# Kernel optimization log

Hardware: AMD Instinct MI355X
Metric: run time of the kernel (lower is better)

Reference implementation:

```python
import jax, jax.numpy as jnp
import numpy as np
from jax import lax

H = 128


def _ema_scan(x):
    # x: [B, T, N, F] -> EMA along T: s_t = 0.9*s_{t-1} + 0.1*x_t
    xt = jnp.moveaxis(x, 1, 0)  # [T, B, N, F]

    def step(s, xi):
        s = s * 0.9 + xi * 0.1
        return s, s

    _, ys = lax.scan(step, jnp.zeros_like(xt[0]), xt)
    return jnp.moveaxis(ys, 0, 1)  # [B, T, N, F]


def setup_inputs() -> dict:
    key = jax.random.key(0)
    k1, k2, k3, k4, k5 = jax.random.split(key, 5)
    B, T, N = 4, 96, 512
    x = jax.random.normal(k1, (B, T, N, H), dtype=jnp.float32)
    s = 1.0 / np.sqrt(H)
    W_exp = jax.random.uniform(k2, (2 * H, H), jnp.float32, -s, s)
    b_exp = jax.random.uniform(k3, (2 * H,), jnp.float32, -s, s)
    W_con = jax.random.uniform(k4, (H, H), jnp.float32, -s, s)
    b_con = jax.random.uniform(k5, (H,), jnp.float32, -s, s)
    return {"spatial_temporal_representation": x, "W_exp": W_exp, "b_exp": b_exp,
            "W_con": W_con, "b_con": b_con}


def reference(spatial_temporal_representation, W_exp, b_exp, W_con, b_con):
    x = spatial_temporal_representation  # [B,T,N,H]
    expanded = jnp.einsum('btnh,oh->btno', x, W_exp) + b_exp  # [B,T,N,2H]
    state_primary, state_gating = jnp.split(expanded, 2, axis=-1)
    gated_activation = jax.nn.sigmoid(_ema_scan(state_gating))
    out = jnp.einsum('btnh,oh->btno', state_primary * gated_activation, W_con) + b_con
    return out
```

## Files before the change

kernel.cpp:

```cpp
#include <hip/hip_runtime.h>

#define B_DIM 4
#define T_DIM 96
#define N_DIM 512
#define H_DIM 128
#define NH    (N_DIM * H_DIM)

#define WS_WEXP  0
#define WS_WCON  32768
#define WS_L     49152
#define WS_TOTAL 58368

typedef __attribute__((ext_vector_type(8))) short short8;
typedef __attribute__((ext_vector_type(4))) float f32x4;

__device__ __forceinline__ unsigned short f2b_rh(float f) {
    union { float f; unsigned u; } c; c.f = f;
    return (unsigned short)((c.u + 0x8000u) >> 16);
}
__device__ __forceinline__ unsigned pack_bf16_2(float a, float b) {
    union { float f; unsigned u; } ca, cb; ca.f = a; cb.f = b;
    return __builtin_amdgcn_perm(cb.u + 0x8000u, ca.u + 0x8000u, 0x07060302u);
}
__device__ __forceinline__ float u2f(unsigned u) {
    union { unsigned u; float f; } c; c.u = u;
    return c.f;
}

extern "C" __global__ void prep_kernel(const float* __restrict__ Wexp,
                                       const float* __restrict__ Wcon,
                                       unsigned short* __restrict__ ws) {
    int i = blockIdx.x * 256 + threadIdx.x;
    if (i < 32768) {
        ws[WS_WEXP + i] = f2b_rh(Wexp[i]);
    } else if (i < 49152) {
        int j = i - 32768;
        ws[WS_WCON + j] = f2b_rh(Wcon[j]);
    } else if (i < WS_TOTAL) {
        int j = i - 49152;
        int t = j / 96, k = j - t * 96;
        float v = 0.0f;
        if (k <= t) v = 0.1f * __expf((float)(t - k) * -0.1053605157f);
        ws[WS_L + j] = f2b_rh(v);
    }
}

extern "C" __global__ __launch_bounds__(256, 3)
void mamba_fused(const float* __restrict__ x,
                 const unsigned short* __restrict__ ws,
                 const float* __restrict__ b_exp,
                 const float* __restrict__ b_con,
                 float* __restrict__ out)
{
    __shared__ __align__(16) unsigned short gateT[H_DIM * 104];
    __shared__ __align__(16) unsigned short xpg[T_DIM * 136];

    const int tid  = threadIdx.x;
    const int wave = tid >> 6;
    const int lane = tid & 63;
    const int q    = lane >> 4;
    const int l16  = lane & 15;

    const int blk = blockIdx.x;
    const int n   = blk & (N_DIM - 1);
    const int b   = blk >> 9;

    const float* xg = x + ((size_t)b * T_DIM * N_DIM + (size_t)n) * H_DIM;

    {
        const int r2    = lane >> 5;
        const int c     = lane & 31;
        const int rbase = wave * 2 + r2;
        #pragma unroll
        for (int i = 0; i < 12; ++i) {
            const int r = i * 8 + rbase;
            float4 v = *(const float4*)(xg + (size_t)r * NH + c * 4);
            union { unsigned u[2]; ushort4 s; } pk;
            pk.u[0] = pack_bf16_2(v.x, v.y);
            pk.u[1] = pack_bf16_2(v.z, v.w);
            *(ushort4*)&xpg[r * 136 + c * 4] = pk.s;
        }
    }

    short8 wp[2][4], wg[2][4];
    #pragma unroll
    for (int ot = 0; ot < 2; ++ot) {
        const unsigned short* wrp = ws + WS_WEXP + (size_t)((wave * 2 + ot) * 16 + l16) * H_DIM + q * 8;
        #pragma unroll
        for (int k0 = 0; k0 < 4; ++k0) {
            wp[ot][k0] = *(const short8*)(wrp + k0 * 32);
            wg[ot][k0] = *(const short8*)(wrp + 128 * H_DIM + k0 * 32);
        }
    }
    __syncthreads();

    unsigned pacc[2][6][2];

    #pragma unroll
    for (int mt = 0; mt < 6; ++mt) {
        short8 bfr[4];
        #pragma unroll
        for (int k0 = 0; k0 < 4; ++k0)
            bfr[k0] = *(const short8*)&xpg[(mt * 16 + l16) * 136 + k0 * 32 + q * 8];
        f32x4 ap0 = {0.f,0.f,0.f,0.f}, ap1 = {0.f,0.f,0.f,0.f};
        f32x4 ag0 = {0.f,0.f,0.f,0.f}, ag1 = {0.f,0.f,0.f,0.f};
        #pragma unroll
        for (int k0 = 0; k0 < 4; ++k0) {
            ap0 = __builtin_amdgcn_mfma_f32_16x16x32_bf16(wp[0][k0], bfr[k0], ap0, 0, 0, 0);
            ap1 = __builtin_amdgcn_mfma_f32_16x16x32_bf16(wp[1][k0], bfr[k0], ap1, 0, 0, 0);
            ag0 = __builtin_amdgcn_mfma_f32_16x16x32_bf16(wg[0][k0], bfr[k0], ag0, 0, 0, 0);
            ag1 = __builtin_amdgcn_mfma_f32_16x16x32_bf16(wg[1][k0], bfr[k0], ag1, 0, 0, 0);
        }
        pacc[0][mt][0] = pack_bf16_2(ap0[0], ap0[1]);
        pacc[0][mt][1] = pack_bf16_2(ap0[2], ap0[3]);
        pacc[1][mt][0] = pack_bf16_2(ap1[0], ap1[1]);
        pacc[1][mt][1] = pack_bf16_2(ap1[2], ap1[3]);
        unsigned short* gr0 = &gateT[((wave * 2 + 0) * 16 + q * 4) * 104 + mt * 16 + l16];
        gr0[0]       = f2b_rh(ag0[0]);
        gr0[104]     = f2b_rh(ag0[1]);
        gr0[2 * 104] = f2b_rh(ag0[2]);
        gr0[3 * 104] = f2b_rh(ag0[3]);
        unsigned short* gr1 = &gateT[((wave * 2 + 1) * 16 + q * 4) * 104 + mt * 16 + l16];
        gr1[0]       = f2b_rh(ag1[0]);
        gr1[104]     = f2b_rh(ag1[1]);
        gr1[2 * 104] = f2b_rh(ag1[2]);
        gr1[3 * 104] = f2b_rh(ag1[3]);
    }

    asm volatile("s_waitcnt lgkmcnt(0)" ::: "memory");
    __builtin_amdgcn_sched_barrier(0);

    f32x4 eacc[2][6];
    #pragma unroll
    for (int ht = 0; ht < 2; ++ht)
        #pragma unroll
        for (int tt = 0; tt < 6; ++tt)
            eacc[ht][tt] = (f32x4){0.f, 0.f, 0.f, 0.f};
    {
        const unsigned short* wsL = ws + WS_L;
        #pragma unroll
        for (int kf = 0; kf < 3; ++kf) {
            short8 af0 = *(const short8*)&gateT[((wave * 2 + 0) * 16 + l16) * 104 + kf * 32 + q * 8];
            short8 af1 = *(const short8*)&gateT[((wave * 2 + 1) * 16 + l16) * 104 + kf * 32 + q * 8];
            #pragma unroll
            for (int tt = 0; tt < 6; ++tt) {
                if (tt < 2 * kf) continue;
                short8 bf = *(const short8*)(wsL + (size_t)(tt * 16 + l16) * 96 + kf * 32 + q * 8);
                eacc[0][tt] = __builtin_amdgcn_mfma_f32_16x16x32_bf16(af0, bf, eacc[0][tt], 0, 0, 0);
                eacc[1][tt] = __builtin_amdgcn_mfma_f32_16x16x32_bf16(af1, bf, eacc[1][tt], 0, 0, 0);
            }
        }
    }

    short8 wc[2][4];
    float4 bias2[2], bp[2], bgv[2];
    #pragma unroll
    for (int ot = 0; ot < 2; ++ot) {
        const int o = (wave * 2 + ot) * 16;
        const unsigned short* wrc = ws + WS_WCON + (size_t)(o + l16) * H_DIM + q * 8;
        #pragma unroll
        for (int k0 = 0; k0 < 4; ++k0)
            wc[ot][k0] = *(const short8*)(wrc + k0 * 32);
        bias2[ot] = *(const float4*)(b_con + o + q * 4);
        bp[ot]    = *(const float4*)(b_exp + o + q * 4);
        bgv[ot]   = *(const float4*)(b_exp + 128 + o + q * 4);
    }
    __syncthreads();

    #pragma unroll
    for (int ot = 0; ot < 2; ++ot) {
        const int hb = (wave * 2 + ot) * 16 + q * 4;
        #pragma unroll
        for (int tt = 0; tt < 6; ++tt) {
            const int t = tt * 16 + l16;
            const float c = 1.0f - __expf((float)(t + 1) * -0.1053605157f);
            f32x4 s = eacc[ot][tt];
            float sg0 = __fdividef(1.f, 1.f + __expf(-(s[0] + bgv[ot].x * c)));
            float sg1 = __fdividef(1.f, 1.f + __expf(-(s[1] + bgv[ot].y * c)));
            float sg2 = __fdividef(1.f, 1.f + __expf(-(s[2] + bgv[ot].z * c)));
            float sg3 = __fdividef(1.f, 1.f + __expf(-(s[3] + bgv[ot].w * c)));
            unsigned u0 = pacc[ot][tt][0], u1 = pacc[ot][tt][1];
            float p0 = (u2f(u0 << 16)         + bp[ot].x) * sg0;
            float p1 = (u2f(u0 & 0xffff0000u) + bp[ot].y) * sg1;
            float p2 = (u2f(u1 << 16)         + bp[ot].z) * sg2;
            float p3 = (u2f(u1 & 0xffff0000u) + bp[ot].w) * sg3;
            union { unsigned u[2]; ushort4 s; } pk;
            pk.u[0] = pack_bf16_2(p0, p1);
            pk.u[1] = pack_bf16_2(p2, p3);
            *(ushort4*)&xpg[t * 136 + hb] = pk.s;
        }
    }
    __syncthreads();

    float* og = out + ((size_t)b * T_DIM * N_DIM + (size_t)n) * H_DIM;
    #pragma unroll
    for (int mt = 0; mt < 6; ++mt) {
        short8 bfr[4];
        const unsigned short* prow = &xpg[(mt * 16 + l16) * 136];
        #pragma unroll
        for (int k0 = 0; k0 < 4; ++k0)
            bfr[k0] = *(const short8*)(prow + k0 * 32 + q * 8);
        const int t = mt * 16 + l16;
        #pragma unroll
        for (int ot = 0; ot < 2; ++ot) {
            f32x4 acc = {0.f, 0.f, 0.f, 0.f};
            #pragma unroll
            for (int k0 = 0; k0 < 4; ++k0)
                acc = __builtin_amdgcn_mfma_f32_16x16x32_bf16(wc[ot][k0], bfr[k0], acc, 0, 0, 0);
            const int o = (wave * 2 + ot) * 16 + q * 4;
            float4 v;
            v.x = acc[0] + bias2[ot].x;
            v.y = acc[1] + bias2[ot].y;
            v.z = acc[2] + bias2[ot].z;
            v.w = acc[3] + bias2[ot].w;
            *(float4*)(og + (size_t)t * NH + o) = v;
        }
    }
}

extern "C" void kernel_launch(void* const* d_in, const int* in_sizes, int n_in,
                              void* d_out, int out_size, void* d_ws, size_t ws_size,
                              hipStream_t stream) {
    const float* x     = (const float*)d_in[0];
    const float* W_exp = (const float*)d_in[1];
    const float* b_exp = (const float*)d_in[2];
    const float* W_con = (const float*)d_in[3];
    const float* b_con = (const float*)d_in[4];
    float* out = (float*)d_out;
    unsigned short* ws = (unsigned short*)d_ws;

    hipLaunchKernelGGL(prep_kernel, dim3(WS_TOTAL / 256), dim3(256), 0, stream,
                       W_exp, W_con, ws);
    hipLaunchKernelGGL(mamba_fused, dim3(B_DIM * N_DIM), dim3(256), 0, stream,
                       x, ws, b_exp, b_con, out);
}
```

Measured before the change: 224.7 us.

## Interleave gate projection with EMA matmul using small per-wave swizzled LDS buffer

```diff
diff --git a/kernel.cpp b/kernel.cpp
--- a/kernel.cpp
+++ b/kernel.cpp
@@ -45,15 +45,15 @@
     }
 }
 
-extern "C" __global__ __launch_bounds__(256, 3)
+extern "C" __global__ __launch_bounds__(256, 4)
 void mamba_fused(const float* __restrict__ x,
                  const unsigned short* __restrict__ ws,
                  const float* __restrict__ b_exp,
                  const float* __restrict__ b_con,
                  float* __restrict__ out)
 {
-    __shared__ __align__(16) unsigned short gateT[H_DIM * 104];
     __shared__ __align__(16) unsigned short xpg[T_DIM * 136];
+    __shared__ __align__(16) unsigned short gbuf[4 * 32 * 40];
 
     const int tid  = threadIdx.x;
     const int wave = tid >> 6;
@@ -95,60 +95,62 @@
     __syncthreads();
 
     unsigned pacc[2][6][2];
-
-    #pragma unroll
-    for (int mt = 0; mt < 6; ++mt) {
-        short8 bfr[4];
-        #pragma unroll
-        for (int k0 = 0; k0 < 4; ++k0)
-            bfr[k0] = *(const short8*)&xpg[(mt * 16 + l16) * 136 + k0 * 32 + q * 8];
-        f32x4 ap0 = {0.f,0.f,0.f,0.f}, ap1 = {0.f,0.f,0.f,0.f};
-        f32x4 ag0 = {0.f,0.f,0.f,0.f}, ag1 = {0.f,0.f,0.f,0.f};
-        #pragma unroll
-        for (int k0 = 0; k0 < 4; ++k0) {
-            ap0 = __builtin_amdgcn_mfma_f32_16x16x32_bf16(wp[0][k0], bfr[k0], ap0, 0, 0, 0);
-            ap1 = __builtin_amdgcn_mfma_f32_16x16x32_bf16(wp[1][k0], bfr[k0], ap1, 0, 0, 0);
-            ag0 = __builtin_amdgcn_mfma_f32_16x16x32_bf16(wg[0][k0], bfr[k0], ag0, 0, 0, 0);
-            ag1 = __builtin_amdgcn_mfma_f32_16x16x32_bf16(wg[1][k0], bfr[k0], ag1, 0, 0, 0);
-        }
-        pacc[0][mt][0] = pack_bf16_2(ap0[0], ap0[1]);
-        pacc[0][mt][1] = pack_bf16_2(ap0[2], ap0[3]);
-        pacc[1][mt][0] = pack_bf16_2(ap1[0], ap1[1]);
-        pacc[1][mt][1] = pack_bf16_2(ap1[2], ap1[3]);
-        unsigned short* gr0 = &gateT[((wave * 2 + 0) * 16 + q * 4) * 104 + mt * 16 + l16];
-        gr0[0]       = f2b_rh(ag0[0]);
-        gr0[104]     = f2b_rh(ag0[1]);
-        gr0[2 * 104] = f2b_rh(ag0[2]);
-        gr0[3 * 104] = f2b_rh(ag0[3]);
-        unsigned short* gr1 = &gateT[((wave * 2 + 1) * 16 + q * 4) * 104 + mt * 16 + l16];
-        gr1[0]       = f2b_rh(ag1[0]);
-        gr1[104]     = f2b_rh(ag1[1]);
-        gr1[2 * 104] = f2b_rh(ag1[2]);
-        gr1[3 * 104] = f2b_rh(ag1[3]);
-    }
-
-    asm volatile("s_waitcnt lgkmcnt(0)" ::: "memory");
-    __builtin_amdgcn_sched_barrier(0);
-
     f32x4 eacc[2][6];
     #pragma unroll
     for (int ht = 0; ht < 2; ++ht)
         #pragma unroll
         for (int tt = 0; tt < 6; ++tt)
             eacc[ht][tt] = (f32x4){0.f, 0.f, 0.f, 0.f};
-    {
-        const unsigned short* wsL = ws + WS_L;
-        #pragma unroll
-        for (int kf = 0; kf < 3; ++kf) {
-            short8 af0 = *(const short8*)&gateT[((wave * 2 + 0) * 16 + l16) * 104 + kf * 32 + q * 8];
-            short8 af1 = *(const short8*)&gateT[((wave * 2 + 1) * 16 + l16) * 104 + kf * 32 + q * 8];
+
+    const unsigned short* wsL = ws + WS_L;
+    unsigned short* gw = gbuf + wave * 1280;
+
+    #pragma unroll
+    for (int kf = 0; kf < 3; ++kf) {
+        #pragma unroll
+        for (int m01 = 0; m01 < 2; ++m01) {
+            const int mt = kf * 2 + m01;
+            short8 bfr[4];
             #pragma unroll
-            for (int tt = 0; tt < 6; ++tt) {
-                if (tt < 2 * kf) continue;
-                short8 bf = *(const short8*)(wsL + (size_t)(tt * 16 + l16) * 96 + kf * 32 + q * 8);
-                eacc[0][tt] = __builtin_amdgcn_mfma_f32_16x16x32_bf16(af0, bf, eacc[0][tt], 0, 0, 0);
-                eacc[1][tt] = __builtin_amdgcn_mfma_f32_16x16x32_bf16(af1, bf, eacc[1][tt], 0, 0, 0);
+            for (int k0 = 0; k0 < 4; ++k0)
+                bfr[k0] = *(const short8*)&xpg[(mt * 16 + l16) * 136 + k0 * 32 + q * 8];
+            f32x4 ap0 = {0.f,0.f,0.f,0.f}, ap1 = {0.f,0.f,0.f,0.f};
+            f32x4 ag0 = {0.f,0.f,0.f,0.f}, ag1 = {0.f,0.f,0.f,0.f};
+            #pragma unroll
+            for (int k0 = 0; k0 < 4; ++k0) {
+                ap0 = __builtin_amdgcn_mfma_f32_16x16x32_bf16(wp[0][k0], bfr[k0], ap0, 0, 0, 0);
+                ap1 = __builtin_amdgcn_mfma_f32_16x16x32_bf16(wp[1][k0], bfr[k0], ap1, 0, 0, 0);
+                ag0 = __builtin_amdgcn_mfma_f32_16x16x32_bf16(wg[0][k0], bfr[k0], ag0, 0, 0, 0);
+                ag1 = __builtin_amdgcn_mfma_f32_16x16x32_bf16(wg[1][k0], bfr[k0], ag1, 0, 0, 0);
             }
+            pacc[0][mt][0] = pack_bf16_2(ap0[0], ap0[1]);
+            pacc[0][mt][1] = pack_bf16_2(ap0[2], ap0[3]);
+            pacc[1][mt][0] = pack_bf16_2(ap1[0], ap1[1]);
+            pacc[1][mt][1] = pack_bf16_2(ap1[2], ap1[3]);
+            const int cw = (m01 * 16 + l16) ^ ((q >> 1) << 4);
+            unsigned short* g0 = gw + (q * 4) * 40 + cw;
+            unsigned short* g1 = g0 + 16 * 40;
+            g0[0]      = f2b_rh(ag0[0]);
+            g0[40]     = f2b_rh(ag0[1]);
+            g0[2 * 40] = f2b_rh(ag0[2]);
+            g0[3 * 40] = f2b_rh(ag0[3]);
+            g1[0]      = f2b_rh(ag1[0]);
+            g1[40]     = f2b_rh(ag1[1]);
+            g1[2 * 40] = f2b_rh(ag1[2]);
+            g1[3 * 40] = f2b_rh(ag1[3]);
+        }
+        asm volatile("s_waitcnt lgkmcnt(0)" ::: "memory");
+        __builtin_amdgcn_sched_barrier(0);
+
+        const int cr = (q * 8) ^ ((l16 >> 3) << 4);
+        short8 af0 = *(const short8*)&gw[l16 * 40 + cr];
+        short8 af1 = *(const short8*)&gw[(16 + l16) * 40 + cr];
+        #pragma unroll
+        for (int tt = 0; tt < 6; ++tt) {
+            if (tt < 2 * kf) continue;
+            short8 bf = *(const short8*)(wsL + (size_t)(tt * 16 + l16) * 96 + kf * 32 + q * 8);
+            eacc[0][tt] = __builtin_amdgcn_mfma_f32_16x16x32_bf16(af0, bf, eacc[0][tt], 0, 0, 0);
+            eacc[1][tt] = __builtin_amdgcn_mfma_f32_16x16x32_bf16(af1, bf, eacc[1][tt], 0, 0, 0);
         }
     }
 
```

Result: slower. 261.3 us (+16.3%).

## Load x directly into MFMA fragments and merge LDS buffers for higher occupancy

Applied to the files above, without the earlier changes.

```diff
diff --git a/kernel.cpp b/kernel.cpp
--- a/kernel.cpp
+++ b/kernel.cpp
@@ -45,15 +45,14 @@
     }
 }
 
-extern "C" __global__ __launch_bounds__(256, 3)
+extern "C" __global__ __launch_bounds__(256, 4)
 void mamba_fused(const float* __restrict__ x,
                  const unsigned short* __restrict__ ws,
                  const float* __restrict__ b_exp,
                  const float* __restrict__ b_con,
                  float* __restrict__ out)
 {
-    __shared__ __align__(16) unsigned short gateT[H_DIM * 104];
-    __shared__ __align__(16) unsigned short xpg[T_DIM * 136];
+    __shared__ __align__(16) unsigned short gpg[128 * 104];
 
     const int tid  = threadIdx.x;
     const int wave = tid >> 6;
@@ -67,21 +66,6 @@
 
     const float* xg = x + ((size_t)b * T_DIM * N_DIM + (size_t)n) * H_DIM;
 
-    {
-        const int r2    = lane >> 5;
-        const int c     = lane & 31;
-        const int rbase = wave * 2 + r2;
-        #pragma unroll
-        for (int i = 0; i < 12; ++i) {
-            const int r = i * 8 + rbase;
-            float4 v = *(const float4*)(xg + (size_t)r * NH + c * 4);
-            union { unsigned u[2]; ushort4 s; } pk;
-            pk.u[0] = pack_bf16_2(v.x, v.y);
-            pk.u[1] = pack_bf16_2(v.z, v.w);
-            *(ushort4*)&xpg[r * 136 + c * 4] = pk.s;
-        }
-    }
-
     short8 wp[2][4], wg[2][4];
     #pragma unroll
     for (int ot = 0; ot < 2; ++ot) {
@@ -92,16 +76,24 @@
             wg[ot][k0] = *(const short8*)(wrp + 128 * H_DIM + k0 * 32);
         }
     }
-    __syncthreads();
 
     unsigned pacc[2][6][2];
 
     #pragma unroll
     for (int mt = 0; mt < 6; ++mt) {
+        const float* xrow = xg + (size_t)(mt * 16 + l16) * NH + q * 8;
         short8 bfr[4];
         #pragma unroll
-        for (int k0 = 0; k0 < 4; ++k0)
-            bfr[k0] = *(const short8*)&xpg[(mt * 16 + l16) * 136 + k0 * 32 + q * 8];
+        for (int k0 = 0; k0 < 4; ++k0) {
+            float4 v0 = *(const float4*)(xrow + k0 * 32);
+            float4 v1 = *(const float4*)(xrow + k0 * 32 + 4);
+            union { unsigned u[4]; short8 s; } p;
+            p.u[0] = pack_bf16_2(v0.x, v0.y);
+            p.u[1] = pack_bf16_2(v0.z, v0.w);
+            p.u[2] = pack_bf16_2(v1.x, v1.y);
+            p.u[3] = pack_bf16_2(v1.z, v1.w);
+            bfr[k0] = p.s;
+        }
         f32x4 ap0 = {0.f,0.f,0.f,0.f}, ap1 = {0.f,0.f,0.f,0.f};
         f32x4 ag0 = {0.f,0.f,0.f,0.f}, ag1 = {0.f,0.f,0.f,0.f};
         #pragma unroll
@@ -115,12 +107,12 @@
         pacc[0][mt][1] = pack_bf16_2(ap0[2], ap0[3]);
         pacc[1][mt][0] = pack_bf16_2(ap1[0], ap1[1]);
         pacc[1][mt][1] = pack_bf16_2(ap1[2], ap1[3]);
-        unsigned short* gr0 = &gateT[((wave * 2 + 0) * 16 + q * 4) * 104 + mt * 16 + l16];
+        unsigned short* gr0 = &gpg[((wave * 2 + 0) * 16 + q * 4) * 104 + mt * 16 + l16];
         gr0[0]       = f2b_rh(ag0[0]);
         gr0[104]     = f2b_rh(ag0[1]);
         gr0[2 * 104] = f2b_rh(ag0[2]);
         gr0[3 * 104] = f2b_rh(ag0[3]);
-        unsigned short* gr1 = &gateT[((wave * 2 + 1) * 16 + q * 4) * 104 + mt * 16 + l16];
+        unsigned short* gr1 = &gpg[((wave * 2 + 1) * 16 + q * 4) * 104 + mt * 16 + l16];
         gr1[0]       = f2b_rh(ag1[0]);
         gr1[104]     = f2b_rh(ag1[1]);
         gr1[2 * 104] = f2b_rh(ag1[2]);
@@ -140,8 +132,8 @@
         const unsigned short* wsL = ws + WS_L;
         #pragma unroll
         for (int kf = 0; kf < 3; ++kf) {
-            short8 af0 = *(const short8*)&gateT[((wave * 2 + 0) * 16 + l16) * 104 + kf * 32 + q * 8];
-            short8 af1 = *(const short8*)&gateT[((wave * 2 + 1) * 16 + l16) * 104 + kf * 32 + q * 8];
+            short8 af0 = *(const short8*)&gpg[((wave * 2 + 0) * 16 + l16) * 104 + kf * 32 + q * 8];
+            short8 af1 = *(const short8*)&gpg[((wave * 2 + 1) * 16 + l16) * 104 + kf * 32 + q * 8];
             #pragma unroll
             for (int tt = 0; tt < 6; ++tt) {
                 if (tt < 2 * kf) continue;
@@ -152,19 +144,18 @@
         }
     }
 
-    short8 wc[2][4];
-    float4 bias2[2], bp[2], bgv[2];
+    float4 bp[2], bgv[2];
     #pragma unroll
     for (int ot = 0; ot < 2; ++ot) {
         const int o = (wave * 2 + ot) * 16;
-        const unsigned short* wrc = ws + WS_WCON + (size_t)(o + l16) * H_DIM + q * 8;
-        #pragma unroll
-        for (int k0 = 0; k0 < 4; ++k0)
-            wc[ot][k0] = *(const short8*)(wrc + k0 * 32);
-        bias2[ot] = *(const float4*)(b_con + o + q * 4);
-        bp[ot]    = *(const float4*)(b_exp + o + q * 4);
-        bgv[ot]   = *(const float4*)(b_exp + 128 + o + q * 4);
-    }
+        bp[ot]  = *(const float4*)(b_exp + o + q * 4);
+        bgv[ot] = *(const float4*)(b_exp + 128 + o + q * 4);
+    }
+    float cfac[6];
+    #pragma unroll
+    for (int tt = 0; tt < 6; ++tt)
+        cfac[tt] = 1.0f - __expf((float)(tt * 16 + l16 + 1) * -0.1053605157f);
+
     __syncthreads();
 
     #pragma unroll
@@ -173,12 +164,11 @@
         #pragma unroll
         for (int tt = 0; tt < 6; ++tt) {
             const int t = tt * 16 + l16;
-            const float c = 1.0f - __expf((float)(t + 1) * -0.1053605157f);
             f32x4 s = eacc[ot][tt];
-            float sg0 = __fdividef(1.f, 1.f + __expf(-(s[0] + bgv[ot].x * c)));
-            float sg1 = __fdividef(1.f, 1.f + __expf(-(s[1] + bgv[ot].y * c)));
-            float sg2 = __fdividef(1.f, 1.f + __expf(-(s[2] + bgv[ot].z * c)));
-            float sg3 = __fdividef(1.f, 1.f + __expf(-(s[3] + bgv[ot].w * c)));
+            float sg0 = __fdividef(1.f, 1.f + __expf(-(s[0] + bgv[ot].x * cfac[tt])));
+            float sg1 = __fdividef(1.f, 1.f + __expf(-(s[1] + bgv[ot].y * cfac[tt])));
+            float sg2 = __fdividef(1.f, 1.f + __expf(-(s[2] + bgv[ot].z * cfac[tt])));
+            float sg3 = __fdividef(1.f, 1.f + __expf(-(s[3] + bgv[ot].w * cfac[tt])));
             unsigned u0 = pacc[ot][tt][0], u1 = pacc[ot][tt][1];
             float p0 = (u2f(u0 << 16)         + bp[ot].x) * sg0;
             float p1 = (u2f(u0 & 0xffff0000u) + bp[ot].y) * sg1;
@@ -187,8 +177,20 @@
             union { unsigned u[2]; ushort4 s; } pk;
             pk.u[0] = pack_bf16_2(p0, p1);
             pk.u[1] = pack_bf16_2(p2, p3);
-            *(ushort4*)&xpg[t * 136 + hb] = pk.s;
-        }
+            *(ushort4*)&gpg[t * 136 + hb] = pk.s;
+        }
+    }
+
+    short8 wc[2][4];
+    float4 bias2[2];
+    #pragma unroll
+    for (int ot = 0; ot < 2; ++ot) {
+        const int o = (wave * 2 + ot) * 16;
+        const unsigned short* wrc = ws + WS_WCON + (size_t)(o + l16) * H_DIM + q * 8;
+        #pragma unroll
+        for (int k0 = 0; k0 < 4; ++k0)
+            wc[ot][k0] = *(const short8*)(wrc + k0 * 32);
+        bias2[ot] = *(const float4*)(b_con + o + q * 4);
     }
     __syncthreads();
 
@@ -196,7 +198,7 @@
     #pragma unroll
     for (int mt = 0; mt < 6; ++mt) {
         short8 bfr[4];
-        const unsigned short* prow = &xpg[(mt * 16 + l16) * 136];
+        const unsigned short* prow = &gpg[(mt * 16 + l16) * 136];
         #pragma unroll
         for (int k0 = 0; k0 < 4; ++k0)
             bfr[k0] = *(const short8*)(prow + k0 * 32 + q * 8);
```

Measured after the change: 239.4 us. 6.5% more time.
